# Performance work log

Measured on AMD Instinct MI355X. Metric: run time of the kernel, lower is better.

Reference implementation:

```python
import jax, jax.numpy as jnp
import numpy as np

B, N, E, H = 64, 512, 1024, 16
DH = E // H


def setup_inputs() -> dict:
    key = jax.random.key(0)
    ks = jax.random.split(key, 5)
    x = jax.random.normal(ks[0], (B, N, E), dtype=jnp.float32)
    # Linear weights stored as [in, out] (transpose of torch's [out, in]); y = x @ W + b
    Wqkv = jax.random.normal(ks[1], (E, 3 * E), dtype=jnp.float32) * 0.02
    bqkv = jnp.zeros((3 * E,), dtype=jnp.float32)
    Wproj = jax.random.normal(ks[2], (E, E), dtype=jnp.float32) * 0.02
    bproj = jnp.zeros((E,), dtype=jnp.float32)
    adj = jax.random.randint(ks[3], (N, N), 0, 2, dtype=jnp.int32)
    return {"x": x, "Wqkv": Wqkv, "bqkv": bqkv, "Wproj": Wproj, "bproj": bproj, "adj": adj}


def reference(x, Wqkv, bqkv, Wproj, bproj, adj):
    b, n, e = x.shape
    h, dh = H, e // H
    # fused QKV projection
    qkv = (x @ Wqkv + bqkv).reshape(b, n, 3, h, dh)
    qkv = jnp.transpose(qkv, (2, 0, 3, 1, 4))  # [3, B, H, N, Dh]
    q, k, v = qkv[0], qkv[1], qkv[2]
    # adjacency mask with self-loops (adj + eye, then bool), broadcast over B, H
    mask = (adj + jnp.eye(n, dtype=adj.dtype)) > 0  # [N, N]
    scale = 1.0 / jnp.sqrt(jnp.asarray(dh, dtype=x.dtype))
    scores = jnp.einsum("bhnd,bhmd->bhnm", q, k) * scale  # [B, H, N, N]
    scores = jnp.where(mask[None, None], scores, jnp.finfo(scores.dtype).min)
    attn = jax.nn.softmax(scores, axis=-1)
    y = jnp.einsum("bhnm,bhmd->bhnd", attn, v)  # [B, H, N, Dh]
    y = jnp.transpose(y, (0, 2, 1, 3)).reshape(b, n, e)
    return y @ Wproj + bproj
```

## Files before the change

kernel.cpp:

```cpp
#include <hip/hip_runtime.h>
#include <hip/hip_bf16.h>

#define Bz 64
#define Nz 512
#define Ez 1024
#define Hz 16
#define DHz 64

static constexpr int MROWS = Bz * Nz;
static constexpr int NQKV  = 3 * Ez;

typedef __attribute__((ext_vector_type(8))) short bf16x8_t;
typedef __attribute__((ext_vector_type(4))) float f32x4_t;
typedef __attribute__((ext_vector_type(16))) float f32x16_t;
typedef __attribute__((ext_vector_type(4))) unsigned u32x4_t;

union FragU { bf16x8_t h; u32x4_t u; };

__device__ __forceinline__ unsigned short f2bf(float f) {
    union { float f; unsigned u; } v; v.f = f;
    unsigned r = v.u + 0x7FFFu + ((v.u >> 16) & 1u);
    return (unsigned short)(r >> 16);
}
__device__ __forceinline__ float bf2f(unsigned short h) {
    union { unsigned u; float f; } v; v.u = ((unsigned)h) << 16;
    return v.f;
}
__device__ __forceinline__ unsigned packbf(float a, float b) {
    union { float f; unsigned u; } x, y; x.f = a; y.f = b;
    return ((x.u + 0x8000u) >> 16) | ((y.u + 0x8000u) & 0xFFFF0000u);
}

__device__ __forceinline__ void async16(const unsigned short* g, unsigned short* l) {
    __builtin_amdgcn_global_load_lds(
        (const __attribute__((address_space(1))) void*)g,
        (__attribute__((address_space(3))) void*)l, 16, 0, 0);
}

__global__ void cvt_f32_bf16(const float* __restrict__ in,
                             unsigned short* __restrict__ out, int n4) {
    int id = blockIdx.x * blockDim.x + threadIdx.x;
    int stride = gridDim.x * blockDim.x;
    for (int i = id; i < n4; i += stride) {
        float4 f = ((const float4*)in)[i];
        ushort4 o;
        o.x = f2bf(f.x); o.y = f2bf(f.y); o.z = f2bf(f.z); o.w = f2bf(f.w);
        ((ushort4*)out)[i] = o;
    }
}

__global__ __launch_bounds__(256)
void cvt_transpose(const float* __restrict__ in,
                   unsigned short* __restrict__ out,
                   int K, int Ncols) {
    int n  = blockIdx.x * 256 + threadIdx.x;
    int k0 = blockIdx.y * 8;
    bf16x8_t o;
#pragma unroll
    for (int j = 0; j < 8; j++)
        o[j] = (short)f2bf(in[(long)(k0 + j) * Ncols + n]);
    *(bf16x8_t*)&out[(long)n * K + k0] = o;
}

__global__ void build_adjm(const int* __restrict__ adj,
                           unsigned long long* __restrict__ adjm) {
    int id = blockIdx.x * blockDim.x + threadIdx.x;
    int n = id >> 3, w = id & 7;
    const int4* r4 = (const int4*)(adj + (long)n * Nz + w * 64);
    unsigned long long m = 0;
#pragma unroll
    for (int c = 0; c < 16; c++) {
        int4 v = r4[c];
        unsigned long long bits =
            (unsigned long long)(v.x != 0) | ((unsigned long long)(v.y != 0) << 1) |
            ((unsigned long long)(v.z != 0) << 2) | ((unsigned long long)(v.w != 0) << 3);
        m |= bits << (c * 4);
    }
    if ((n >> 6) == w) m |= 1ull << (n & 63);
    adjm[id] = m;
}

template<bool OUT_BF16>
__device__ __forceinline__
void gemm_body(const unsigned short* __restrict__ A,
               const unsigned short* __restrict__ BT,
               const float* __restrict__ bias,
               void* __restrict__ C,
               int M, int Ncols, int K) {
    const int tid  = threadIdx.x;
    const int wave = tid >> 6;
    const int lane = tid & 63;
    const int wm = (wave >> 1) * 64;
    const int wn = (wave & 1) * 64;
    const int m32 = lane & 31;
    const int kh  = lane >> 5;

    const int rowBase = blockIdx.y * 128;
    const int colBase = blockIdx.x * 128;

    __shared__ __align__(16) unsigned short As[128][64];
    __shared__ __align__(16) unsigned short Bs[128][64];

    f32x16_t acc[2][2];
#pragma unroll
    for (int i = 0; i < 2; i++)
#pragma unroll
        for (int j = 0; j < 2; j++)
#pragma unroll
            for (int r = 0; r < 16; r++)
                acc[i][j][r] = 0.0f;

    const unsigned short* pa[4];
    const unsigned short* pb[4];
#pragma unroll
    for (int cc = 0; cc < 4; cc++) {
        int s = tid + cc * 256;
        int r = s >> 3;
        int c = (s & 7) ^ (r & 7);
        pa[cc] = &A [(long)(rowBase + r) * K + c * 8];
        pb[cc] = &BT[(long)(colBase + r) * K + c * 8];
    }
    const int fsw = m32 & 7;

    for (int k0 = 0; k0 < K; k0 += 64) {
        __syncthreads();
#pragma unroll
        for (int cc = 0; cc < 4; cc++) {
            async16(pa[cc] + k0, (unsigned short*)As + (size_t)(cc * 64 + wave * 16) * 32);
            async16(pb[cc] + k0, (unsigned short*)Bs + (size_t)(cc * 64 + wave * 16) * 32);
        }
        __syncthreads();

        bf16x8_t af[2][4], bfr[2][4];
#pragma unroll
        for (int kc = 0; kc < 4; kc++) {
            int p = (kc * 2 + kh) ^ fsw;
#pragma unroll
            for (int t = 0; t < 2; t++) {
                af[t][kc]  = *(bf16x8_t*)&As[wm + t * 32 + m32][p * 8];
                bfr[t][kc] = *(bf16x8_t*)&Bs[wn + t * 32 + m32][p * 8];
            }
        }
#pragma unroll
        for (int kc = 0; kc < 4; kc++)
#pragma unroll
            for (int i = 0; i < 2; i++)
#pragma unroll
                for (int j = 0; j < 2; j++)
                    acc[i][j] = __builtin_amdgcn_mfma_f32_32x32x16_bf16(
                        af[i][kc], bfr[j][kc], acc[i][j], 0, 0, 0);
    }

#pragma unroll
    for (int j = 0; j < 2; j++) {
        int col = colBase + wn + j * 32 + m32;
        float bv = bias[col];
#pragma unroll
        for (int i = 0; i < 2; i++) {
#pragma unroll
            for (int reg = 0; reg < 16; reg++) {
                int row = rowBase + wm + i * 32 + (reg & 3) + 8 * (reg >> 2) + 4 * kh;
                float v = acc[i][j][reg] + bv;
                if (OUT_BF16)
                    ((unsigned short*)C)[(long)row * Ncols + col] = f2bf(v);
                else
                    ((float*)C)[(long)row * Ncols + col] = v;
            }
        }
    }
}

__global__ __launch_bounds__(256)
void gemm_qkv(const unsigned short* __restrict__ A,
              const unsigned short* __restrict__ BT,
              const float* __restrict__ bias,
              void* __restrict__ C, int M, int Ncols, int K) {
    gemm_body<true>(A, BT, bias, C, M, Ncols, K);
}

__global__ __launch_bounds__(256)
void gemm_proj(const unsigned short* __restrict__ A,
               const unsigned short* __restrict__ BT,
               const float* __restrict__ bias,
               void* __restrict__ C, int M, int Ncols, int K) {
    gemm_body<false>(A, BT, bias, C, M, Ncols, K);
}

__global__ __launch_bounds__(512, 2)
void attn_mfma(const unsigned short* __restrict__ qkv,
               const unsigned long long* __restrict__ adjm,
               unsigned short* __restrict__ y)
{
    const int h = blockIdx.x;
    const int b = blockIdx.y;
    const int tid  = threadIdx.x;
    const int lane = tid & 63;
    const int w    = tid >> 6;
    const int l16  = lane & 15;
    const int q    = lane >> 4;

    __shared__ __align__(16) unsigned short Ks[512][64];
    __shared__ __align__(16) unsigned short Vt[64][512];

    const long rowB = (long)b * Nz;
    const unsigned short* base = qkv + rowB * NQKV;

    for (int idx = tid; idx < 4096; idx += 512) {
        int n = idx >> 3, cc = idx & 7;
        *(bf16x8_t*)&Ks[n][(cc ^ (n & 7)) * 8] =
            *(const bf16x8_t*)&base[(long)n * NQKV + Ez + h * DHz + cc * 8];
    }
    {
        int tp = tid & 255, dh = tid >> 8;
        int n0 = tp * 2;
        bf16x8_t va[4], vb[4];
#pragma unroll
        for (int c = 0; c < 4; c++) {
            va[c] = *(const bf16x8_t*)&base[(long)n0 * NQKV + 2 * Ez + h * DHz + dh * 32 + c * 8];
            vb[c] = *(const bf16x8_t*)&base[(long)(n0 + 1) * NQKV + 2 * Ez + h * DHz + dh * 32 + c * 8];
        }
        unsigned short* vt = &Vt[0][0];
#pragma unroll
        for (int dd = 0; dd < 32; dd++) {
            int d = dh * 32 + dd;
            unsigned lo = (unsigned)(unsigned short)va[dd >> 3][dd & 7];
            unsigned hi = (unsigned)(unsigned short)vb[dd >> 3][dd & 7];
            int cp = (n0 >> 3) ^ (d & 7);
            *(unsigned*)&vt[d * 512 + cp * 8 + (n0 & 7)] = lo | (hi << 16);
        }
    }
    FragU qf[4][2];
#pragma unroll
    for (int mt = 0; mt < 4; mt++)
#pragma unroll
        for (int kc = 0; kc < 2; kc++)
            qf[mt][kc].h = *(const bf16x8_t*)&base[(long)(w * 64 + mt * 16 + l16) * NQKV
                                                   + h * DHz + kc * 32 + q * 8];
    __syncthreads();

    f32x4_t oacc[4][4];
#pragma unroll
    for (int mt = 0; mt < 4; mt++)
#pragma unroll
        for (int dt = 0; dt < 4; dt++) {
            f32x4_t z = {0.0f, 0.0f, 0.0f, 0.0f};
            oacc[mt][dt] = z;
        }
    float rsum[4] = {0.0f, 0.0f, 0.0f, 0.0f};
    unsigned long long wm[4];

    for (int ct = 0; ct < 16; ct++) {
        const int j0 = ct * 32;
        if ((ct & 1) == 0) {
#pragma unroll
            for (int mt = 0; mt < 4; mt++)
                wm[mt] = adjm[(size_t)(w * 64 + mt * 16 + l16) * 8 + (ct >> 1)];
        }
        bf16x8_t kf[2][2];
#pragma unroll
        for (int jt = 0; jt < 2; jt++)
#pragma unroll
            for (int kc = 0; kc < 2; kc++)
                kf[jt][kc] = *(const bf16x8_t*)
                    &Ks[j0 + jt * 16 + l16][((kc * 4 + q) ^ (l16 & 7)) * 8];

        f32x4_t tacc[2][4];
        __builtin_amdgcn_s_setprio(1);
#pragma unroll
        for (int jt = 0; jt < 2; jt++)
#pragma unroll
            for (int mt = 0; mt < 4; mt++) {
                f32x4_t z = {0.0f, 0.0f, 0.0f, 0.0f};
                z = __builtin_amdgcn_mfma_f32_16x16x32_bf16(kf[jt][0], qf[mt][0].h, z, 0, 0, 0);
                tacc[jt][mt] = __builtin_amdgcn_mfma_f32_16x16x32_bf16(kf[jt][1], qf[mt][1].h, z, 0, 0, 0);
            }
        __builtin_amdgcn_s_setprio(0);

        unsigned pk[2][4][2];
#pragma unroll
        for (int jt = 0; jt < 2; jt++)
#pragma unroll
            for (int mt = 0; mt < 4; mt++) {
                float e[4];
#pragma unroll
                for (int r = 0; r < 4; r++) {
                    int jrel = (ct & 1) * 32 + jt * 16 + q * 4 + r;
                    bool bit = (wm[mt] >> jrel) & 1ull;
                    float ev = bit ? __expf(tacc[jt][mt][r] * 0.125f) : 0.0f;
                    e[r] = ev;
                    rsum[mt] += ev;
                }
                pk[jt][mt][0] = packbf(e[0], e[1]);
                pk[jt][mt][1] = packbf(e[2], e[3]);
            }

        bf16x8_t vf[4];
#pragma unroll
        for (int dt = 0; dt < 4; dt++) {
            int d = dt * 16 + l16;
            int cp = (ct * 4 + q) ^ (l16 & 7);
            vf[dt] = *(const bf16x8_t*)&(&Vt[0][0])[d * 512 + cp * 8];
        }

#pragma unroll
        for (int mt = 0; mt < 4; mt++) {
            FragU pf;
#pragma unroll
            for (int p = 0; p < 4; p++) {
                int srcl = ((lane & 16) << 1) | ((p & 2) << 3) | l16;
                unsigned a0 = (unsigned)__shfl((int)pk[0][mt][p & 1], srcl);
                unsigned a1 = (unsigned)__shfl((int)pk[1][mt][p & 1], srcl);
                pf.u[p] = (lane & 32) ? a1 : a0;
            }
            __builtin_amdgcn_s_setprio(1);
#pragma unroll
            for (int dt = 0; dt < 4; dt++)
                oacc[mt][dt] = __builtin_amdgcn_mfma_f32_16x16x32_bf16(
                    pf.h, vf[dt], oacc[mt][dt], 0, 0, 0);
            __builtin_amdgcn_s_setprio(0);
        }
    }

#pragma unroll
    for (int mt = 0; mt < 4; mt++) {
        float s = rsum[mt];
        s += __shfl_xor(s, 16);
        s += __shfl_xor(s, 32);
#pragma unroll
        for (int r = 0; r < 4; r++) {
            float rs = __shfl(s, (lane & 48) | (q * 4) | r);
            float inv = 1.0f / rs;
            int row = w * 64 + mt * 16 + q * 4 + r;
#pragma unroll
            for (int dt = 0; dt < 4; dt++)
                y[(rowB + row) * Ez + h * DHz + dt * 16 + l16] =
                    f2bf(oacc[mt][dt][r] * inv);
        }
    }
}

extern "C" void kernel_launch(void* const* d_in, const int* in_sizes, int n_in,
                              void* d_out, int out_size, void* d_ws, size_t ws_size,
                              hipStream_t stream) {
    const float* x     = (const float*)d_in[0];
    const float* Wqkv  = (const float*)d_in[1];
    const float* bqkv  = (const float*)d_in[2];
    const float* Wproj = (const float*)d_in[3];
    const float* bproj = (const float*)d_in[4];
    const int*   adj   = (const int*)d_in[5];
    float* out = (float*)d_out;

    char* ws = (char*)d_ws;
    unsigned short* xb     = (unsigned short*)(ws);
    unsigned short* qkv    = (unsigned short*)(ws + 67108864);
    unsigned short* WqkvT  = (unsigned short*)(ws + 268435456);
    unsigned short* WprojT = (unsigned short*)(ws + 274726912);
    unsigned long long* adjm = (unsigned long long*)(ws + 276824064);
    unsigned short* yb = xb;

    cvt_f32_bf16<<<8192, 256, 0, stream>>>(x, xb, (Bz * Nz * Ez) / 4);
    cvt_transpose<<<dim3(NQKV / 256, Ez / 8), 256, 0, stream>>>(Wqkv, WqkvT, Ez, NQKV);
    cvt_transpose<<<dim3(Ez / 256, Ez / 8), 256, 0, stream>>>(Wproj, WprojT, Ez, Ez);
    build_adjm<<<16, 256, 0, stream>>>(adj, adjm);

    gemm_qkv<<<dim3(NQKV / 128, MROWS / 128), 256, 0, stream>>>(
        xb, WqkvT, bqkv, qkv, MROWS, NQKV, Ez);

    attn_mfma<<<dim3(Hz, Bz), 512, 0, stream>>>(qkv, adjm, yb);

    gemm_proj<<<dim3(Ez / 128, MROWS / 128), 256, 0, stream>>>(
        yb, WprojT, bproj, out, MROWS, Ez, Ez);
}
```

Measured before the change: 746.0 us.

## Double-buffer K/V tiles in attention kernel to cut LDS and overlap loads

Result: slower. 2.246 ms (+201.1%).

```diff
diff --git a/kernel.cpp b/kernel.cpp
--- a/kernel.cpp
+++ b/kernel.cpp
@@ -186,7 +186,7 @@
     gemm_body<false>(A, BT, bias, C, M, Ncols, K);
 }
 
-__global__ __launch_bounds__(512, 2)
+__global__ __launch_bounds__(512, 4)
 void attn_mfma(const unsigned short* __restrict__ qkv,
                const unsigned long long* __restrict__ adjm,
                unsigned short* __restrict__ y)
@@ -199,36 +199,22 @@
     const int l16  = lane & 15;
     const int q    = lane >> 4;
 
-    __shared__ __align__(16) unsigned short Ks[512][64];
-    __shared__ __align__(16) unsigned short Vt[64][512];
+    __shared__ __align__(16) unsigned short Ks[2][128][64];
+    __shared__ __align__(16) unsigned short Vt[2][64][128];
 
     const long rowB = (long)b * Nz;
     const unsigned short* base = qkv + rowB * NQKV;
 
-    for (int idx = tid; idx < 4096; idx += 512) {
-        int n = idx >> 3, cc = idx & 7;
-        *(bf16x8_t*)&Ks[n][(cc ^ (n & 7)) * 8] =
-            *(const bf16x8_t*)&base[(long)n * NQKV + Ez + h * DHz + cc * 8];
-    }
-    {
-        int tp = tid & 255, dh = tid >> 8;
-        int n0 = tp * 2;
-        bf16x8_t va[4], vb[4];
-#pragma unroll
-        for (int c = 0; c < 4; c++) {
-            va[c] = *(const bf16x8_t*)&base[(long)n0 * NQKV + 2 * Ez + h * DHz + dh * 32 + c * 8];
-            vb[c] = *(const bf16x8_t*)&base[(long)(n0 + 1) * NQKV + 2 * Ez + h * DHz + dh * 32 + c * 8];
-        }
-        unsigned short* vt = &Vt[0][0];
-#pragma unroll
-        for (int dd = 0; dd < 32; dd++) {
-            int d = dh * 32 + dd;
-            unsigned lo = (unsigned)(unsigned short)va[dd >> 3][dd & 7];
-            unsigned hi = (unsigned)(unsigned short)vb[dd >> 3][dd & 7];
-            int cp = (n0 >> 3) ^ (d & 7);
-            *(unsigned*)&vt[d * 512 + cp * 8 + (n0 & 7)] = lo | (hi << 16);
-        }
-    }
+    const int kn0 = tid >> 3;
+    const int kn1 = (tid + 512) >> 3;
+    const int kcc = tid & 7;
+    const int vnl = (tid & 63) * 2;
+    const int vdh = tid >> 6;
+
+#define KLOAD(kt, n) (*(const bf16x8_t*)&base[(long)((kt) * 128 + (n)) * NQKV + Ez + h * DHz + kcc * 8])
+#define VLOAD(kt, n) (*(const bf16x8_t*)&base[(long)((kt) * 128 + (n)) * NQKV + 2 * Ez + h * DHz + vdh * 8])
+#define KWRITE(bf, n, v) (*(bf16x8_t*)&Ks[bf][n][(kcc ^ ((n) & 7)) * 8] = (v))
+
     FragU qf[4][2];
 #pragma unroll
     for (int mt = 0; mt < 4; mt++)
@@ -236,6 +222,20 @@
         for (int kc = 0; kc < 2; kc++)
             qf[mt][kc].h = *(const bf16x8_t*)&base[(long)(w * 64 + mt * 16 + l16) * NQKV
                                                    + h * DHz + kc * 32 + q * 8];
+
+    {
+        bf16x8_t ka = KLOAD(0, kn0), kb = KLOAD(0, kn1);
+        bf16x8_t va = VLOAD(0, vnl), vb = VLOAD(0, vnl + 1);
+        KWRITE(0, kn0, ka); KWRITE(0, kn1, kb);
+#pragma unroll
+        for (int dd = 0; dd < 8; dd++) {
+            int d = vdh * 8 + dd;
+            unsigned lo = (unsigned)(unsigned short)va[dd];
+            unsigned hi = (unsigned)(unsigned short)vb[dd];
+            int cp = (vnl >> 3) ^ (d & 7);
+            *(unsigned*)&Vt[0][d][cp * 8 + (vnl & 7)] = lo | (hi << 16);
+        }
+    }
     __syncthreads();
 
     f32x4_t oacc[4][4];
@@ -249,77 +249,104 @@
     float rsum[4] = {0.0f, 0.0f, 0.0f, 0.0f};
     unsigned long long wm[4];
 
-    for (int ct = 0; ct < 16; ct++) {
-        const int j0 = ct * 32;
-        if ((ct & 1) == 0) {
-#pragma unroll
-            for (int mt = 0; mt < 4; mt++)
-                wm[mt] = adjm[(size_t)(w * 64 + mt * 16 + l16) * 8 + (ct >> 1)];
-        }
-        bf16x8_t kf[2][2];
-#pragma unroll
-        for (int jt = 0; jt < 2; jt++)
-#pragma unroll
-            for (int kc = 0; kc < 2; kc++)
-                kf[jt][kc] = *(const bf16x8_t*)
-                    &Ks[j0 + jt * 16 + l16][((kc * 4 + q) ^ (l16 & 7)) * 8];
-
-        f32x4_t tacc[2][4];
-        __builtin_amdgcn_s_setprio(1);
-#pragma unroll
-        for (int jt = 0; jt < 2; jt++)
+    for (int kt = 0; kt < 4; kt++) {
+        const int buf = kt & 1;
+
+        bf16x8_t ka, kb, va, vb;
+        if (kt < 3) {
+            ka = KLOAD(kt + 1, kn0); kb = KLOAD(kt + 1, kn1);
+            va = VLOAD(kt + 1, vnl); vb = VLOAD(kt + 1, vnl + 1);
+        }
+
+#pragma unroll
+        for (int lt = 0; lt < 4; lt++) {
+            const int ct = kt * 4 + lt;
+            if ((ct & 1) == 0) {
+#pragma unroll
+                for (int mt = 0; mt < 4; mt++)
+                    wm[mt] = adjm[(size_t)(w * 64 + mt * 16 + l16) * 8 + (ct >> 1)];
+            }
+            bf16x8_t kf[2][2];
+#pragma unroll
+            for (int jt = 0; jt < 2; jt++)
+#pragma unroll
+                for (int kc = 0; kc < 2; kc++)
+                    kf[jt][kc] = *(const bf16x8_t*)
+                        &Ks[buf][lt * 32 + jt * 16 + l16][((kc * 4 + q) ^ (l16 & 7)) * 8];
+
+            f32x4_t tacc[2][4];
+            __builtin_amdgcn_s_setprio(1);
+#pragma unroll
+            for (int jt = 0; jt < 2; jt++)
+#pragma unroll
+                for (int mt = 0; mt < 4; mt++) {
+                    f32x4_t z = {0.0f, 0.0f, 0.0f, 0.0f};
+                    z = __builtin_amdgcn_mfma_f32_16x16x32_bf16(kf[jt][0], qf[mt][0].h, z, 0, 0, 0);
+                    tacc[jt][mt] = __builtin_amdgcn_mfma_f32_16x16x32_bf16(kf[jt][1], qf[mt][1].h, z, 0, 0, 0);
+                }
+            __builtin_amdgcn_s_setprio(0);
+
+            unsigned pk[2][4][2];
+#pragma unroll
+            for (int jt = 0; jt < 2; jt++)
+#pragma unroll
+                for (int mt = 0; mt < 4; mt++) {
+                    float e[4];
+#pragma unroll
+                    for (int r = 0; r < 4; r++) {
+                        int jrel = (ct & 1) * 32 + jt * 16 + q * 4 + r;
+                        bool bit = (wm[mt] >> jrel) & 1ull;
+                        float ev = bit ? __expf(tacc[jt][mt][r] * 0.125f) : 0.0f;
+                        e[r] = ev;
+                        rsum[mt] += ev;
+                    }
+                    pk[jt][mt][0] = packbf(e[0], e[1]);
+                    pk[jt][mt][1] = packbf(e[2], e[3]);
+                }
+
+            bf16x8_t vf[4];
+#pragma unroll
+            for (int dt = 0; dt < 4; dt++) {
+                int d = dt * 16 + l16;
+                int cp = (lt * 4 + q) ^ (l16 & 7);
+                vf[dt] = *(const bf16x8_t*)&Vt[buf][d][cp * 8];
+            }
+
 #pragma unroll
             for (int mt = 0; mt < 4; mt++) {
-                f32x4_t z = {0.0f, 0.0f, 0.0f, 0.0f};
-                z = __builtin_amdgcn_mfma_f32_16x16x32_bf16(kf[jt][0], qf[mt][0].h, z, 0, 0, 0);
-                tacc[jt][mt] = __builtin_amdgcn_mfma_f32_16x16x32_bf16(kf[jt][1], qf[mt][1].h, z, 0, 0, 0);
-            }
-        __builtin_amdgcn_s_setprio(0);
-
-        unsigned pk[2][4][2];
-#pragma unroll
-        for (int jt = 0; jt < 2; jt++)
-#pragma unroll
-            for (int mt = 0; mt < 4; mt++) {
-                float e[4];
-#pragma unroll
-                for (int r = 0; r < 4; r++) {
-                    int jrel = (ct & 1) * 32 + jt * 16 + q * 4 + r;
-                    bool bit = (wm[mt] >> jrel) & 1ull;
-                    float ev = bit ? __expf(tacc[jt][mt][r] * 0.125f) : 0.0f;
-                    e[r] = ev;
-                    rsum[mt] += ev;
+                FragU pf;
+#pragma unroll
+                for (int p = 0; p < 4; p++) {
+                    int srcl = ((lane & 16) << 1) | ((p & 2) << 3) | l16;
+                    unsigned a0 = (unsigned)__shfl((int)pk[0][mt][p & 1], srcl);
+                    unsigned a1 = (unsigned)__shfl((int)pk[1][mt][p & 1], srcl);
+                    pf.u[p] = (lane & 32) ? a1 : a0;
                 }
-                pk[jt][mt][0] = packbf(e[0], e[1]);
-                pk[jt][mt][1] = packbf(e[2], e[3]);
-            }
-
-        bf16x8_t vf[4];
-#pragma unroll
-        for (int dt = 0; dt < 4; dt++) {
-            int d = dt * 16 + l16;
-            int cp = (ct * 4 + q) ^ (l16 & 7);
-            vf[dt] = *(const bf16x8_t*)&(&Vt[0][0])[d * 512 + cp * 8];
-        }
-
-#pragma unroll
-        for (int mt = 0; mt < 4; mt++) {
-            FragU pf;
-#pragma unroll
-            for (int p = 0; p < 4; p++) {
-                int srcl = ((lane & 16) << 1) | ((p & 2) << 3) | l16;
-                unsigned a0 = (unsigned)__shfl((int)pk[0][mt][p & 1], srcl);
-                unsigned a1 = (unsigned)__shfl((int)pk[1][mt][p & 1], srcl);
-                pf.u[p] = (lane & 32) ? a1 : a0;
-            }
-            __builtin_amdgcn_s_setprio(1);
-#pragma unroll
-            for (int dt = 0; dt < 4; dt++)
-                oacc[mt][dt] = __builtin_amdgcn_mfma_f32_16x16x32_bf16(
-                    pf.h, vf[dt], oacc[mt][dt], 0, 0, 0);
-            __builtin_amdgcn_s_setprio(0);
-        }
-    }
+                __builtin_amdgcn_s_setprio(1);
+#pragma unroll
+                for (int dt = 0; dt < 4; dt++)
+                    oacc[mt][dt] = __builtin_amdgcn_mfma_f32_16x16x32_bf16(
+                        pf.h, vf[dt], oacc[mt][dt], 0, 0, 0);
+                __builtin_amdgcn_s_setprio(0);
+            }
+        }
+
+        if (kt < 3) {
+            KWRITE(buf ^ 1, kn0, ka); KWRITE(buf ^ 1, kn1, kb);
+#pragma unroll
+            for (int dd = 0; dd < 8; dd++) {
+                int d = vdh * 8 + dd;
+                unsigned lo = (unsigned)(unsigned short)va[dd];
+                unsigned hi = (unsigned)(unsigned short)vb[dd];
+                int cp = (vnl >> 3) ^ (d & 7);
+                *(unsigned*)&Vt[buf ^ 1][d][cp * 8 + (vnl & 7)] = lo | (hi << 16);
+            }
+            __syncthreads();
+        }
+    }
+#undef KLOAD
+#undef VLOAD
+#undef KWRITE
 
 #pragma unroll
     for (int mt = 0; mt < 4; mt++) {
```
